# Kernel tuning notes

Measured on AMD Instinct MI355X. Metric: run time of the kernel, lower is better.

Reference implementation:

```python
import jax, jax.numpy as jnp
import numpy as np

EMBED_DIM = 512
N_QUERY = 4096
N_PROTO = 1024


def setup_inputs() -> dict:
    key = jax.random.key(0)
    k_q, k_p, k_wmu = jax.random.split(key, 3)
    d = EMBED_DIM
    bound = (6.0 / (d + d)) ** 0.5
    return {
        "query_features": jax.random.normal(k_q, (N_QUERY, d), dtype=jnp.float32),
        "prototypes": jax.random.normal(k_p, (N_PROTO, d), dtype=jnp.float32),
        "weight_mu": jax.random.uniform(k_wmu, (d, d), dtype=jnp.float32, minval=-bound, maxval=bound),
        "weight_rho": jnp.full((d, d), -3.0, dtype=jnp.float32),
        "bias_mu": jnp.zeros((d,), dtype=jnp.float32),
        "bias_rho": jnp.full((d,), 0.01, dtype=jnp.float32),
        "n_samples": 10,
    }


def reference(query_features, prototypes, weight_mu, weight_rho, bias_mu, bias_rho, n_samples):
    d = weight_mu.shape[0]
    # softplus reparameterization (same each iteration in the original loop)
    weight_sigma = jnp.log1p(jnp.exp(weight_rho))  # [d, d]
    bias_sigma = jnp.log1p(jnp.exp(bias_rho))      # [d]
    # batched MC weight/bias samples: [S, d, d] and [S, d]
    key = jax.random.key(42)
    kw, kb = jax.random.split(key)
    eps_w = jax.random.normal(kw, (n_samples, d, d), dtype=weight_mu.dtype)
    eps_b = jax.random.normal(kb, (n_samples, d), dtype=bias_mu.dtype)
    w = weight_mu[None] + weight_sigma[None] * eps_w   # [S, d, d]
    b = bias_mu[None] + bias_sigma[None] * eps_b       # [S, d]
    # F.linear(x, W_sample.T, b) == x @ W_sample + b
    tq = jnp.einsum('qd,sde->sqe', query_features, w) + b[:, None, :]  # [S, Q, d]
    # cdist via ||a||^2 + ||b||^2 - 2 a.b
    sq_q = jnp.sum(tq * tq, axis=-1)                    # [S, Q]
    sq_p = jnp.sum(prototypes * prototypes, axis=-1)    # [P]
    cross = jnp.einsum('sqe,pe->sqp', tq, prototypes)   # [S, Q, P]
    sqd = sq_q[:, :, None] + sq_p[None, None, :] - 2.0 * cross
    dists = jnp.sqrt(jnp.maximum(sqd, 1e-12))           # [S, Q, P]
    mean_distance = jnp.mean(dists, axis=0)
    uncertainty = jnp.std(dists, axis=0, ddof=1)        # torch.std is unbiased
    return mean_distance, uncertainty
```

## Files before the change

### kernel.cpp

```cpp
#include <hip/hip_runtime.h>
#include <stdint.h>

#define NS 10
#define DIM 512
#define NQ 4096
#define NP 1024

typedef unsigned short ushort_t;
typedef __bf16 bf16el_t;
typedef bf16el_t bf16x8 __attribute__((ext_vector_type(8)));
typedef float floatx4 __attribute__((ext_vector_type(4)));

__host__ __device__ __forceinline__ uint32_t rotl32(uint32_t x, int r) {
  return (x << r) | (x >> (32 - r));
}

__host__ __device__ __forceinline__ void threefry2x32(uint32_t k0, uint32_t k1,
                                                      uint32_t x0, uint32_t x1,
                                                      uint32_t* o0, uint32_t* o1) {
  uint32_t ks2 = k0 ^ k1 ^ 0x1BD11BDAu;
  x0 += k0; x1 += k1;
#define TF_R(r) { x0 += x1; x1 = rotl32(x1, r); x1 ^= x0; }
  TF_R(13) TF_R(15) TF_R(26) TF_R(6)   x0 += k1;  x1 += ks2 + 1u;
  TF_R(17) TF_R(29) TF_R(16) TF_R(24)  x0 += ks2; x1 += k0 + 2u;
  TF_R(13) TF_R(15) TF_R(26) TF_R(6)   x0 += k0;  x1 += k1 + 3u;
  TF_R(17) TF_R(29) TF_R(16) TF_R(24)  x0 += k1;  x1 += ks2 + 4u;
  TF_R(13) TF_R(15) TF_R(26) TF_R(6)   x0 += ks2; x1 += k0 + 5u;
#undef TF_R
  *o0 = x0; *o1 = x1;
}

__device__ __forceinline__ uint32_t jax_random_bits(uint32_t k0, uint32_t k1, uint32_t idx) {
  uint32_t o0, o1;
  threefry2x32(k0, k1, 0u, idx, &o0, &o1);
  return o0 ^ o1;
}

__device__ __forceinline__ float erfinvf_xla(float x) {
  float w = -log1pf(-x * x);
  float p;
  if (w < 5.0f) {
    w -= 2.5f;
    p = 2.81022636e-08f;
    p = fmaf(p, w, 3.43273939e-07f);
    p = fmaf(p, w, -3.5233877e-06f);
    p = fmaf(p, w, -4.39150654e-06f);
    p = fmaf(p, w, 0.00021858087f);
    p = fmaf(p, w, -0.00125372503f);
    p = fmaf(p, w, -0.00417768164f);
    p = fmaf(p, w, 0.246640727f);
    p = fmaf(p, w, 1.50140941f);
  } else {
    w = sqrtf(w) - 3.0f;
    p = -0.000200214257f;
    p = fmaf(p, w, 0.000100950558f);
    p = fmaf(p, w, 0.00134934322f);
    p = fmaf(p, w, -0.00367342844f);
    p = fmaf(p, w, 0.00573950773f);
    p = fmaf(p, w, -0.0076224613f);
    p = fmaf(p, w, 0.00943887047f);
    p = fmaf(p, w, 1.00167406f);
    p = fmaf(p, w, 2.83297682f);
  }
  return p * x;
}

__device__ __forceinline__ float jax_bits_to_normal(uint32_t bits) {
  float f = __uint_as_float((bits >> 9) | 0x3F800000u) - 1.0f;
  float u = f * 2.0f - 0.99999994f;
  u = fmaxf(u, -0.99999994f);
  return 1.41421356f * erfinvf_xla(u);
}

__device__ __forceinline__ float softplusf(float x) { return log1pf(expf(x)); }

__device__ __forceinline__ float bf2f(ushort_t u) {
  return __uint_as_float(((uint32_t)u) << 16);
}
__device__ __forceinline__ ushort_t f2bf(float f) {
  uint32_t u = __float_as_uint(f);
  u += 0x7FFFu + ((u >> 16) & 1u);
  return (ushort_t)(u >> 16);
}

__device__ __forceinline__ void gll16(const void* g, void* l) {
  __builtin_amdgcn_global_load_lds(
      (const __attribute__((address_space(1))) uint32_t*)g,
      (__attribute__((address_space(3))) uint32_t*)l, 16, 0, 0);
}

__global__ __launch_bounds__(256) void prep_kernel(const float* __restrict__ qf,
                                                   const float* __restrict__ pf,
                                                   const float* __restrict__ wmu,
                                                   const float* __restrict__ wrho,
                                                   const float* __restrict__ bmu,
                                                   const float* __restrict__ brho,
                                                   ushort_t* __restrict__ wt,
                                                   ushort_t* __restrict__ qb,
                                                   ushort_t* __restrict__ pb,
                                                   float* __restrict__ sqp,
                                                   float* __restrict__ bvec,
                                                   float* __restrict__ sqq,
                                                   uint32_t kw0, uint32_t kw1,
                                                   uint32_t kb0, uint32_t kb1) {
  const int blk = blockIdx.x;
  const int tid = threadIdx.x;
  if (blk < 10240) {
    uint32_t t = blk * 256u + tid;
    uint32_t s = t >> 18;
    uint32_t r = t & 0x3FFFFu;
    uint32_t e = r >> 9;
    uint32_t k = r & 511u;
    uint32_t eps_idx = (s << 18) | (k << 9) | e;
    uint32_t bits = jax_random_bits(kw0, kw1, eps_idx);
    float n = jax_bits_to_normal(bits);
    uint32_t mi = (k << 9) | e;
    float w = wmu[mi] + softplusf(wrho[mi]) * n;
    wt[t] = f2bf(w);
  } else if (blk < 12288) {
    int i = ((blk - 10240) * 256 + tid) * 4;
    float4 v = *(const float4*)&qf[i];
    uint2 r;
    r.x = (uint32_t)f2bf(v.x) | ((uint32_t)f2bf(v.y) << 16);
    r.y = (uint32_t)f2bf(v.z) | ((uint32_t)f2bf(v.w) << 16);
    *(uint2*)&qb[i] = r;
  } else if (blk < 12544) {
    int p = (blk - 12288) * 4 + (tid >> 6);
    int lane = tid & 63;
    const float* src = pf + p * DIM + lane * 8;
    float4 a = *(const float4*)src;
    float4 b = *(const float4*)(src + 4);
    float vals[8] = {a.x, a.y, a.z, a.w, b.x, b.y, b.z, b.w};
    ushort_t o[8];
    float ss = 0.f;
#pragma unroll
    for (int i = 0; i < 8; ++i) {
      o[i] = f2bf(vals[i]);
      float f = bf2f(o[i]);
      ss += f * f;
    }
    *(uint4*)&pb[p * DIM + lane * 8] = *(const uint4*)o;
#pragma unroll
    for (int off = 32; off; off >>= 1) ss += __shfl_xor(ss, off, 64);
    if (lane == 0) sqp[p] = ss;
  } else if (blk < 12564) {
    uint32_t t2 = (blk - 12544) * 256u + tid;
    uint32_t e = t2 & 511u;
    uint32_t bits = jax_random_bits(kb0, kb1, t2);
    float n = jax_bits_to_normal(bits);
    bvec[t2] = bmu[e] + softplusf(brho[e]) * n;
  } else {
    int i = (blk - 12564) * 256 + tid;
    sqq[i] = 0.f;
  }
}

__global__ __launch_bounds__(256) void gemm_tq_kernel(const ushort_t* __restrict__ qb,
                                                      const ushort_t* __restrict__ wt,
                                                      const float* __restrict__ bvec,
                                                      ushort_t* __restrict__ tq,
                                                      float* __restrict__ sqq) {
  __shared__ __align__(16) ushort_t ls[2 * 128 * 64];
  ushort_t* lsA = ls;
  ushort_t* lsB = ls + 128 * 64;
  const int lane = threadIdx.x & 63;
  const int wave = threadIdx.x >> 6;
  const int wm = wave >> 1, wn = wave & 1;
  const int qBase = blockIdx.x * 128;
  const int eBase = blockIdx.y * 128;
  const int s = blockIdx.z;
  const ushort_t* wbase = wt + (size_t)s * (DIM * DIM);
  const int srow = lane >> 3;
  const int scol = ((lane & 7) ^ srow) * 16;
  const char* gA = (const char*)qb + (size_t)(qBase + wave * 32 + srow) * (DIM * 2) + scol;
  const char* gB = (const char*)wbase + (size_t)(eBase + wave * 32 + srow) * (DIM * 2) + scol;
  char* lA = (char*)&lsA[wave * 32 * 64];
  char* lB = (char*)&lsB[wave * 32 * 64];
  const int cn = lane & 15;
  const int cn7 = cn & 7;
  const int jc = lane >> 4;
  const floatx4 fzero = {0.f, 0.f, 0.f, 0.f};
  floatx4 acc[4][4];
#pragma unroll
  for (int mi = 0; mi < 4; ++mi)
#pragma unroll
    for (int ni = 0; ni < 4; ++ni) acc[mi][ni] = fzero;

  for (int kt = 0; kt < 8; ++kt) {
    __syncthreads();
#pragma unroll
    for (int j = 0; j < 4; ++j) {
      gll16(gA + (size_t)j * 8 * (DIM * 2), lA + j * 1024);
      gll16(gB + (size_t)j * 8 * (DIM * 2), lB + j * 1024);
    }
    gA += 128; gB += 128;
    __syncthreads();
#pragma unroll
    for (int c = 0; c < 8; c += 4) {
      const int po = ((c + jc) ^ cn7) << 3;
      bf16x8 aF[4], bF[4];
#pragma unroll
      for (int mi = 0; mi < 4; ++mi)
        aF[mi] = *(const bf16x8*)&lsA[(wm * 64 + mi * 16 + cn) * 64 + po];
#pragma unroll
      for (int ni = 0; ni < 4; ++ni)
        bF[ni] = *(const bf16x8*)&lsB[(wn * 64 + ni * 16 + cn) * 64 + po];
#pragma unroll
      for (int mi = 0; mi < 4; ++mi)
#pragma unroll
        for (int ni = 0; ni < 4; ++ni)
          acc[mi][ni] = __builtin_amdgcn_mfma_f32_16x16x32_bf16(aF[mi], bF[ni], acc[mi][ni], 0, 0, 0);
    }
  }

  __syncthreads();
  ushort_t* area = ls + wave * 4096;
  float bv[4];
#pragma unroll
  for (int ni = 0; ni < 4; ++ni) bv[ni] = bvec[s * DIM + eBase + wn * 64 + ni * 16 + cn];
  const int jc4 = jc * 4;
#pragma unroll
  for (int mi = 0; mi < 4; ++mi)
#pragma unroll
    for (int ni = 0; ni < 4; ++ni)
#pragma unroll
      for (int r = 0; r < 4; ++r) {
        const int lr = mi * 16 + jc4 + r;
        const int lc = ni * 16 + cn;
        const int off = lr * 64 + (((lc >> 3) ^ (lr & 7)) << 3) + (lc & 7);
        area[off] = f2bf(acc[mi][ni][r] + bv[ni]);
      }
  __syncthreads();
  const int rr = lane >> 3;
  const int ch = lane & 7;
  const int physc = ch ^ rr;
  const size_t tqs = (size_t)s * (NQ * DIM);
#pragma unroll
  for (int pass = 0; pass < 8; ++pass) {
    const int lr = pass * 8 + rr;
    uint4 v = *(const uint4*)&area[lr * 64 + physc * 8];
    uint32_t wsv[4] = {v.x, v.y, v.z, v.w};
    float ss = 0.f;
#pragma unroll
    for (int i = 0; i < 4; ++i) {
      float lo = bf2f((ushort_t)(wsv[i] & 0xFFFFu));
      float hi = bf2f((ushort_t)(wsv[i] >> 16));
      ss += lo * lo + hi * hi;
    }
    ss += __shfl_xor(ss, 1, 64);
    ss += __shfl_xor(ss, 2, 64);
    ss += __shfl_xor(ss, 4, 64);
    const int q = qBase + wm * 64 + lr;
    *(uint4*)&tq[tqs + (size_t)q * DIM + eBase + wn * 64 + ch * 8] = v;
    if (ch == 0) atomicAdd(&sqq[s * NQ + q], ss);
  }
}

__global__ __launch_bounds__(256, 2) void gemm_dist_kernel(const ushort_t* __restrict__ tq,
                                                           const ushort_t* __restrict__ pb,
                                                           const float* __restrict__ sqq,
                                                           const float* __restrict__ sqp,
                                                           float* __restrict__ out) {
  __shared__ __align__(16) ushort_t lsA[2 * 64 * 64];
  __shared__ __align__(16) ushort_t lsB[128 * 64];
  const int lane = threadIdx.x & 63;
  const int wave = threadIdx.x >> 6;
  const int wm = wave >> 1;
  const int wn = wave & 1;
  const int qBase = blockIdx.x * 64;
  const int pBase = blockIdx.y * 128;
  const int srow = lane >> 3;
  const int scol = ((lane & 7) ^ srow) * 16;
  const int cn = lane & 15;
  const int cn7 = cn & 7;
  const int jc = lane >> 4;
  const int rq = jc * 4;
  const floatx4 fzero = {0.f, 0.f, 0.f, 0.f};
  const char* gAb = (const char*)tq + (size_t)(qBase + wave * 16 + srow) * (DIM * 2) + scol;
  const char* gBb = (const char*)pb + (size_t)(pBase + wave * 32 + srow) * (DIM * 2) + scol;
  char* lA0 = (char*)lsA + wave * 2048;
  char* lA1 = (char*)lsA + 8192 + wave * 2048;
  char* lBw = (char*)lsB + wave * 4096;
  int po[2];
#pragma unroll
  for (int c = 0; c < 2; ++c) po[c] = ((c * 4 + jc) ^ cn7) << 3;

  float sum[2][4][4] = {};
  float ssq[2][4][4] = {};
  float sqp_v[4];
#pragma unroll
  for (int ni = 0; ni < 4; ++ni) sqp_v[ni] = sqp[pBase + wn * 64 + ni * 16 + cn];

  for (int s0 = 0; s0 < NS; s0 += 2) {
    floatx4 acc[2][2][4];
#pragma unroll
    for (int sp = 0; sp < 2; ++sp)
#pragma unroll
      for (int mi = 0; mi < 2; ++mi)
#pragma unroll
        for (int ni = 0; ni < 4; ++ni) acc[sp][mi][ni] = fzero;

    const char* gA0 = gAb + (size_t)s0 * (NQ * DIM * 2);
    const char* gA1 = gA0 + (size_t)(NQ * DIM * 2);
    const char* gBk = gBb;
    for (int kt = 0; kt < 8; ++kt) {
      __syncthreads();
#pragma unroll
      for (int j = 0; j < 2; ++j) {
        const size_t gRow = (size_t)j * 8 * (DIM * 2);
        gll16(gA0 + gRow, lA0 + j * 1024);
        gll16(gA1 + gRow, lA1 + j * 1024);
      }
#pragma unroll
      for (int j = 0; j < 4; ++j)
        gll16(gBk + (size_t)j * 8 * (DIM * 2), lBw + j * 1024);
      gA0 += 128; gA1 += 128; gBk += 128;
      __syncthreads();
#pragma unroll
      for (int c = 0; c < 2; ++c) {
        bf16x8 bF[4];
#pragma unroll
        for (int ni = 0; ni < 4; ++ni)
          bF[ni] = *(const bf16x8*)&lsB[(wn * 64 + ni * 16 + cn) * 64 + po[c]];
#pragma unroll
        for (int sp = 0; sp < 2; ++sp) {
          bf16x8 aF[2];
#pragma unroll
          for (int mi = 0; mi < 2; ++mi)
            aF[mi] = *(const bf16x8*)&lsA[sp * 4096 + (wm * 32 + mi * 16 + cn) * 64 + po[c]];
#pragma unroll
          for (int mi = 0; mi < 2; ++mi)
#pragma unroll
            for (int ni = 0; ni < 4; ++ni)
              acc[sp][mi][ni] =
                  __builtin_amdgcn_mfma_f32_16x16x32_bf16(aF[mi], bF[ni], acc[sp][mi][ni], 0, 0, 0);
        }
      }
    }
#pragma unroll
    for (int sp = 0; sp < 2; ++sp) {
      const int s = s0 + sp;
#pragma unroll
      for (int mi = 0; mi < 2; ++mi) {
        float4 aqv = *(const float4*)&sqq[s * NQ + qBase + wm * 32 + mi * 16 + rq];
        float aqa[4] = {aqv.x, aqv.y, aqv.z, aqv.w};
#pragma unroll
        for (int r = 0; r < 4; ++r) {
          float aq = aqa[r];
#pragma unroll
          for (int ni = 0; ni < 4; ++ni) {
            float sqd = fmaxf(fmaf(-2.0f, acc[sp][mi][ni][r], aq + sqp_v[ni]), 1e-12f);
            sum[mi][ni][r] += sqrtf(sqd);
            ssq[mi][ni][r] += sqd;
          }
        }
      }
    }
  }
#pragma unroll
  for (int mi = 0; mi < 2; ++mi)
#pragma unroll
    for (int ni = 0; ni < 4; ++ni)
#pragma unroll
      for (int r = 0; r < 4; ++r) {
        int q = qBase + wm * 32 + mi * 16 + rq + r;
        int p = pBase + wn * 64 + ni * 16 + cn;
        float sm = sum[mi][ni][r];
        float mean = sm * 0.1f;
        float var = (ssq[mi][ni][r] - sm * sm * 0.1f) * (1.0f / 9.0f);
        out[(size_t)q * NP + p] = mean;
        out[(size_t)NQ * NP + (size_t)q * NP + p] = sqrtf(fmaxf(var, 0.0f));
      }
}

extern "C" void kernel_launch(void* const* d_in, const int* in_sizes, int n_in,
                              void* d_out, int out_size, void* d_ws, size_t ws_size,
                              hipStream_t stream) {
  const float* qf   = (const float*)d_in[0];
  const float* pf   = (const float*)d_in[1];
  const float* wmu  = (const float*)d_in[2];
  const float* wrho = (const float*)d_in[3];
  const float* bmu  = (const float*)d_in[4];
  const float* brho = (const float*)d_in[5];
  float* out = (float*)d_out;
  char* ws = (char*)d_ws;
  ushort_t* wt   = (ushort_t*)(ws);
  ushort_t* qb   = (ushort_t*)(ws + 5242880);
  ushort_t* pb   = (ushort_t*)(ws + 9437184);
  float*    bvec = (float*)   (ws + 10485760);
  float*    sqp  = (float*)   (ws + 10506240);
  ushort_t* tq   = (ushort_t*)(ws + 10510336);
  float*    sqq  = (float*)   (ws + 52453376);

  uint32_t kw0, kw1, kb0, kb1;
  threefry2x32(0u, 42u, 0u, 0u, &kw0, &kw1);
  threefry2x32(0u, 42u, 0u, 1u, &kb0, &kb1);

  hipLaunchKernelGGL(prep_kernel, dim3(12724), dim3(256), 0, stream,
                     qf, pf, wmu, wrho, bmu, brho, wt, qb, pb, sqp, bvec, sqq,
                     kw0, kw1, kb0, kb1);
  hipLaunchKernelGGL(gemm_tq_kernel, dim3(32, 4, 10), dim3(256), 0, stream, qb, wt, bvec, tq, sqq);
  hipLaunchKernelGGL(gemm_dist_kernel, dim3(64, 8), dim3(256), 0, stream, tq, pb, sqq, sqp, out);
}
```

Measured before the change: 200.0 us.

## Tile weight sampling through LDS transpose and process four samples per distance pass

The weight-sampling part of the prep kernel now has each block handle a 64x64 tile per sample. It loads mu/rho with float4 reads, generates the normals, and transposes through swizzled shared memory, so wt is written in coalesced 16-byte rows instead of scattered per-element accesses. The distance GEMM now groups samples 4,4,2 instead of pairs, which cuts the number of prototype tile reloads and K-loop barriers. The cost is doubled LDS for the A tiles and a larger accumulator array (32 floatx4), which raises register pressure under launch_bounds(256,2) and may cause spills or lower occupancy.

```diff
diff --git a/kernel.cpp b/kernel.cpp
--- a/kernel.cpp
+++ b/kernel.cpp
@@ -103,29 +103,59 @@
                                                    float* __restrict__ sqq,
                                                    uint32_t kw0, uint32_t kw1,
                                                    uint32_t kb0, uint32_t kb1) {
+  __shared__ __align__(16) ushort_t lsW[64 * 64];
   const int blk = blockIdx.x;
   const int tid = threadIdx.x;
-  if (blk < 10240) {
-    uint32_t t = blk * 256u + tid;
-    uint32_t s = t >> 18;
-    uint32_t r = t & 0x3FFFFu;
-    uint32_t e = r >> 9;
-    uint32_t k = r & 511u;
-    uint32_t eps_idx = (s << 18) | (k << 9) | e;
-    uint32_t bits = jax_random_bits(kw0, kw1, eps_idx);
-    float n = jax_bits_to_normal(bits);
-    uint32_t mi = (k << 9) | e;
-    float w = wmu[mi] + softplusf(wrho[mi]) * n;
-    wt[t] = f2bf(w);
-  } else if (blk < 12288) {
-    int i = ((blk - 10240) * 256 + tid) * 4;
+  if (blk < 640) {
+    const int s = blk >> 6;
+    const int rem = blk & 63;
+    const int k0 = (rem >> 3) * 64;
+    const int e0 = (rem & 7) * 64;
+    const int r = tid >> 2;
+    const int ch = tid & 3;
+    const int kg = k0 + r;
+    const int eg = e0 + ch * 16;
+    const float* mup = wmu + kg * DIM + eg;
+    const float* rhop = wrho + kg * DIM + eg;
+    __align__(16) ushort_t wv[16];
+#pragma unroll
+    for (int v = 0; v < 4; ++v) {
+      float4 m4 = *(const float4*)(mup + v * 4);
+      float4 r4 = *(const float4*)(rhop + v * 4);
+      float ms[4] = {m4.x, m4.y, m4.z, m4.w};
+      float rs[4] = {r4.x, r4.y, r4.z, r4.w};
+#pragma unroll
+      for (int u = 0; u < 4; ++u) {
+        uint32_t e = (uint32_t)(eg + v * 4 + u);
+        uint32_t eps_idx = ((uint32_t)s << 18) | ((uint32_t)kg << 9) | e;
+        float n = jax_bits_to_normal(jax_random_bits(kw0, kw1, eps_idx));
+        wv[v * 4 + u] = f2bf(ms[u] + softplusf(rs[u]) * n);
+      }
+    }
+    ushort_t* lrow = lsW + r * 64;
+    *(uint4*)&lrow[((2 * ch) ^ (r & 7)) << 3]     = *(const uint4*)&wv[0];
+    *(uint4*)&lrow[((2 * ch + 1) ^ (r & 7)) << 3] = *(const uint4*)&wv[8];
+    __syncthreads();
+    const int er = tid >> 2;
+    const int kc = tid & 3;
+    __align__(16) ushort_t ov[16];
+#pragma unroll
+    for (int j = 0; j < 16; ++j) {
+      int k = kc * 16 + j;
+      ov[j] = lsW[k * 64 + ((((er >> 3) ^ (k & 7)) << 3)) + (er & 7)];
+    }
+    ushort_t* orow = wt + (size_t)s * (DIM * DIM) + (size_t)(e0 + er) * DIM + k0 + kc * 16;
+    *(uint4*)&orow[0] = *(const uint4*)&ov[0];
+    *(uint4*)&orow[8] = *(const uint4*)&ov[8];
+  } else if (blk < 2688) {
+    int i = ((blk - 640) * 256 + tid) * 4;
     float4 v = *(const float4*)&qf[i];
     uint2 r;
     r.x = (uint32_t)f2bf(v.x) | ((uint32_t)f2bf(v.y) << 16);
     r.y = (uint32_t)f2bf(v.z) | ((uint32_t)f2bf(v.w) << 16);
     *(uint2*)&qb[i] = r;
-  } else if (blk < 12544) {
-    int p = (blk - 12288) * 4 + (tid >> 6);
+  } else if (blk < 2944) {
+    int p = (blk - 2688) * 4 + (tid >> 6);
     int lane = tid & 63;
     const float* src = pf + p * DIM + lane * 8;
     float4 a = *(const float4*)src;
@@ -143,14 +173,14 @@
 #pragma unroll
     for (int off = 32; off; off >>= 1) ss += __shfl_xor(ss, off, 64);
     if (lane == 0) sqp[p] = ss;
-  } else if (blk < 12564) {
-    uint32_t t2 = (blk - 12544) * 256u + tid;
+  } else if (blk < 2964) {
+    uint32_t t2 = (blk - 2944) * 256u + tid;
     uint32_t e = t2 & 511u;
     uint32_t bits = jax_random_bits(kb0, kb1, t2);
     float n = jax_bits_to_normal(bits);
     bvec[t2] = bmu[e] + softplusf(brho[e]) * n;
   } else {
-    int i = (blk - 12564) * 256 + tid;
+    int i = (blk - 2964) * 256 + tid;
     sqq[i] = 0.f;
   }
 }
@@ -261,7 +291,7 @@
                                                            const float* __restrict__ sqq,
                                                            const float* __restrict__ sqp,
                                                            float* __restrict__ out) {
-  __shared__ __align__(16) ushort_t lsA[2 * 64 * 64];
+  __shared__ __align__(16) ushort_t lsA[4 * 64 * 64];
   __shared__ __align__(16) ushort_t lsB[128 * 64];
   const int lane = threadIdx.x & 63;
   const int wave = threadIdx.x >> 6;
@@ -278,8 +308,7 @@
   const floatx4 fzero = {0.f, 0.f, 0.f, 0.f};
   const char* gAb = (const char*)tq + (size_t)(qBase + wave * 16 + srow) * (DIM * 2) + scol;
   const char* gBb = (const char*)pb + (size_t)(pBase + wave * 32 + srow) * (DIM * 2) + scol;
-  char* lA0 = (char*)lsA + wave * 2048;
-  char* lA1 = (char*)lsA + 8192 + wave * 2048;
+  char* lAw = (char*)lsA + wave * 2048;
   char* lBw = (char*)lsB + wave * 4096;
   int po[2];
 #pragma unroll
@@ -291,30 +320,33 @@
 #pragma unroll
   for (int ni = 0; ni < 4; ++ni) sqp_v[ni] = sqp[pBase + wn * 64 + ni * 16 + cn];
 
-  for (int s0 = 0; s0 < NS; s0 += 2) {
-    floatx4 acc[2][2][4];
-#pragma unroll
-    for (int sp = 0; sp < 2; ++sp)
+  for (int grp = 0; grp < 3; ++grp) {
+    const int sbase = grp * 4;
+    const int gsz = (grp == 2) ? 2 : 4;
+    floatx4 acc[4][2][4];
+#pragma unroll
+    for (int sp = 0; sp < 4; ++sp)
 #pragma unroll
       for (int mi = 0; mi < 2; ++mi)
 #pragma unroll
         for (int ni = 0; ni < 4; ++ni) acc[sp][mi][ni] = fzero;
 
-    const char* gA0 = gAb + (size_t)s0 * (NQ * DIM * 2);
-    const char* gA1 = gA0 + (size_t)(NQ * DIM * 2);
+    const char* gAg = gAb + (size_t)sbase * (NQ * DIM * 2);
     const char* gBk = gBb;
     for (int kt = 0; kt < 8; ++kt) {
       __syncthreads();
 #pragma unroll
-      for (int j = 0; j < 2; ++j) {
-        const size_t gRow = (size_t)j * 8 * (DIM * 2);
-        gll16(gA0 + gRow, lA0 + j * 1024);
-        gll16(gA1 + gRow, lA1 + j * 1024);
-      }
+      for (int sp = 0; sp < 4; ++sp)
+        if (sp < gsz) {
+          const char* gs = gAg + (size_t)sp * (NQ * DIM * 2);
+          char* ls = lAw + sp * 8192;
+          gll16(gs, ls);
+          gll16(gs + (size_t)8 * (DIM * 2), ls + 1024);
+        }
 #pragma unroll
       for (int j = 0; j < 4; ++j)
         gll16(gBk + (size_t)j * 8 * (DIM * 2), lBw + j * 1024);
-      gA0 += 128; gA1 += 128; gBk += 128;
+      gAg += 128; gBk += 128;
       __syncthreads();
 #pragma unroll
       for (int c = 0; c < 2; ++c) {
@@ -323,39 +355,41 @@
         for (int ni = 0; ni < 4; ++ni)
           bF[ni] = *(const bf16x8*)&lsB[(wn * 64 + ni * 16 + cn) * 64 + po[c]];
 #pragma unroll
-        for (int sp = 0; sp < 2; ++sp) {
-          bf16x8 aF[2];
-#pragma unroll
-          for (int mi = 0; mi < 2; ++mi)
-            aF[mi] = *(const bf16x8*)&lsA[sp * 4096 + (wm * 32 + mi * 16 + cn) * 64 + po[c]];
-#pragma unroll
-          for (int mi = 0; mi < 2; ++mi)
-#pragma unroll
-            for (int ni = 0; ni < 4; ++ni)
-              acc[sp][mi][ni] =
-                  __builtin_amdgcn_mfma_f32_16x16x32_bf16(aF[mi], bF[ni], acc[sp][mi][ni], 0, 0, 0);
-        }
+        for (int sp = 0; sp < 4; ++sp)
+          if (sp < gsz) {
+            bf16x8 aF[2];
+#pragma unroll
+            for (int mi = 0; mi < 2; ++mi)
+              aF[mi] = *(const bf16x8*)&lsA[sp * 4096 + (wm * 32 + mi * 16 + cn) * 64 + po[c]];
+#pragma unroll
+            for (int mi = 0; mi < 2; ++mi)
+#pragma unroll
+              for (int ni = 0; ni < 4; ++ni)
+                acc[sp][mi][ni] =
+                    __builtin_amdgcn_mfma_f32_16x16x32_bf16(aF[mi], bF[ni], acc[sp][mi][ni], 0, 0, 0);
+          }
       }
     }
 #pragma unroll
-    for (int sp = 0; sp < 2; ++sp) {
-      const int s = s0 + sp;
-#pragma unroll
-      for (int mi = 0; mi < 2; ++mi) {
-        float4 aqv = *(const float4*)&sqq[s * NQ + qBase + wm * 32 + mi * 16 + rq];
-        float aqa[4] = {aqv.x, aqv.y, aqv.z, aqv.w};
-#pragma unroll
-        for (int r = 0; r < 4; ++r) {
-          float aq = aqa[r];
-#pragma unroll
-          for (int ni = 0; ni < 4; ++ni) {
-            float sqd = fmaxf(fmaf(-2.0f, acc[sp][mi][ni][r], aq + sqp_v[ni]), 1e-12f);
-            sum[mi][ni][r] += sqrtf(sqd);
-            ssq[mi][ni][r] += sqd;
+    for (int sp = 0; sp < 4; ++sp)
+      if (sp < gsz) {
+        const int s = sbase + sp;
+#pragma unroll
+        for (int mi = 0; mi < 2; ++mi) {
+          float4 aqv = *(const float4*)&sqq[s * NQ + qBase + wm * 32 + mi * 16 + rq];
+          float aqa[4] = {aqv.x, aqv.y, aqv.z, aqv.w};
+#pragma unroll
+          for (int r = 0; r < 4; ++r) {
+            float aq = aqa[r];
+#pragma unroll
+            for (int ni = 0; ni < 4; ++ni) {
+              float sqd = fmaxf(fmaf(-2.0f, acc[sp][mi][ni][r], aq + sqp_v[ni]), 1e-12f);
+              sum[mi][ni][r] += sqrtf(sqd);
+              ssq[mi][ni][r] += sqd;
+            }
           }
         }
       }
-    }
   }
 #pragma unroll
   for (int mi = 0; mi < 2; ++mi)
@@ -396,7 +430,7 @@
   threefry2x32(0u, 42u, 0u, 0u, &kw0, &kw1);
   threefry2x32(0u, 42u, 0u, 1u, &kb0, &kb1);
 
-  hipLaunchKernelGGL(prep_kernel, dim3(12724), dim3(256), 0, stream,
+  hipLaunchKernelGGL(prep_kernel, dim3(3124), dim3(256), 0, stream,
                      qf, pf, wmu, wrho, bmu, brho, wt, qb, pb, sqp, bvec, sqq,
                      kw0, kw1, kb0, kb1);
   hipLaunchKernelGGL(gemm_tq_kernel, dim3(32, 4, 10), dim3(256), 0, stream, qb, wt, bvec, tq, sqq);
```

After: 197.1 us. No clear change (-1.5%).
